# Kernel optimization log

Hardware: AMD Instinct MI355X
Metric: run time of the kernel (lower is better)

Reference implementation:

```python
import jax, jax.numpy as jnp
import numpy as np

NUM_HEADS = 16


def setup_inputs() -> dict:
    key = jax.random.key(0)
    ks = jax.random.split(key, 5)
    B, S, D = 2, 2048, 1024
    scale = 0.02
    return {
        "x": jax.random.normal(ks[0], (B, S, D), dtype=jnp.float32),
        "Wq": jax.random.normal(ks[1], (D, D), dtype=jnp.float32) * scale,
        "Wk": jax.random.normal(ks[2], (D, D), dtype=jnp.float32) * scale,
        "Wv": jax.random.normal(ks[3], (D, D), dtype=jnp.float32) * scale,
        "Wo": jax.random.normal(ks[4], (D, D), dtype=jnp.float32) * scale,
        "bo": jnp.zeros((D,), dtype=jnp.float32),
    }


def reference(x, Wq, Wk, Wv, Wo, bo):
    B, S, D = x.shape
    H = NUM_HEADS
    Dh = D // H
    # project and split heads -> [B, H, S, Dh]
    q = (x @ Wq).reshape(B, S, H, Dh).transpose(0, 2, 1, 3)
    k = (x @ Wk).reshape(B, S, H, Dh).transpose(0, 2, 1, 3)
    v = (x @ Wv).reshape(B, S, H, Dh).transpose(0, 2, 1, 3)
    # full causal attention scores [B, H, S, S]
    scores = jnp.einsum("bhqd,bhkd->bhqk", q, k)
    causal_mask = jnp.triu(jnp.ones((S, S), dtype=bool), k=1)
    scores = jnp.where(causal_mask, -jnp.inf, scores)
    attn = jax.nn.softmax(scores / jnp.sqrt(jnp.float32(Dh)), axis=-1)
    ctx = jnp.einsum("bhqk,bhkd->bhqd", attn, v)
    ctx = ctx.transpose(0, 2, 1, 3).reshape(B, S, D)
    return ctx @ Wo + bo
```

## Files before the change

kernel.cpp:

```cpp
#include <hip/hip_runtime.h>
#include <hip/hip_bf16.h>
#include <math.h>

typedef __bf16 bf16_t;
typedef bf16_t bf16x4 __attribute__((ext_vector_type(4)));
typedef bf16_t bf16x8 __attribute__((ext_vector_type(8)));
typedef float f32x4 __attribute__((ext_vector_type(4)));
typedef unsigned int u32;
typedef u32 u32x2 __attribute__((ext_vector_type(2)));
typedef u32 u32x4 __attribute__((ext_vector_type(4)));

#define MFMA16(a, b, c) __builtin_amdgcn_mfma_f32_16x16x32_bf16(a, b, c, 0, 0, 0)
#define NEG_BIG (-1e30f)
#define QSCALE 0.18033688f

#define GLL16(gp, lp)                                                          \
    __builtin_amdgcn_global_load_lds(                                          \
        (const __attribute__((address_space(1))) unsigned int*)(gp),           \
        (__attribute__((address_space(3))) unsigned int*)(lp), 16, 0, 0)


__global__ __launch_bounds__(256) void prep(const float* __restrict__ x,
                                            const float* __restrict__ Wq,
                                            const float* __restrict__ Wk,
                                            const float* __restrict__ Wv,
                                            const float* __restrict__ Wo,
                                            bf16_t* __restrict__ Xb,
                                            bf16_t* __restrict__ WTqkv,
                                            bf16_t* __restrict__ WoT) {
    __shared__ float tile[32][33];
    const int z = blockIdx.z;
    const int tx = threadIdx.x, ty = threadIdx.y;
    if (z == 4) {
        int i0 = (((blockIdx.y * 32 + blockIdx.x) * 256) + ty * 32 + tx) * 4;
        for (int j = 0; j < 4; j++) {
            int i = i0 + j * 1048576;
            float4 v = *(const float4*)(x + i);
            Xb[i + 0] = (bf16_t)v.x;
            Xb[i + 1] = (bf16_t)v.y;
            Xb[i + 2] = (bf16_t)v.z;
            Xb[i + 3] = (bf16_t)v.w;
        }
    } else {
        const float* W = (z == 0) ? Wq : (z == 1) ? Wk : (z == 2) ? Wv : Wo;
        bf16_t* WT = (z < 3) ? (WTqkv + (size_t)z * 1048576) : WoT;
        int bx = blockIdx.x * 32, by = blockIdx.y * 32;
        for (int i = 0; i < 32; i += 8)
            tile[ty + i][tx] = W[(size_t)(by + ty + i) * 1024 + bx + tx];
        __syncthreads();
        for (int i = 0; i < 32; i += 8)
            WT[(size_t)(bx + ty + i) * 1024 + by + tx] = (bf16_t)tile[tx][ty + i];
    }
}

__global__ __launch_bounds__(256) void gemm_qkv(const bf16_t* __restrict__ X,
                                                const bf16_t* __restrict__ WT,
                                                bf16_t* __restrict__ Qd,
                                                bf16_t* __restrict__ Kd,
                                                bf16_t* __restrict__ Vd) {
    __shared__ bf16_t AsmF[2][128 * 64];
    __shared__ bf16_t BsmF[2][128 * 64];
    const int bid = blockIdx.x;
    const int logical = (bid & 7) * 96 + (bid >> 3);
    const int which = logical >> 8;
    const int rem = logical & 255;
    const bf16_t* Wt = WT + (size_t)which * 1024 * 1024;
    const int bm = (rem >> 3) * 128;
    const int bn = (rem & 7) * 128;
    const int tid = threadIdx.x;
    const int wave = tid >> 6, lane = tid & 63;
    const int wm = (wave >> 1) * 64, wn = (wave & 1) * 64;
    const int col = lane & 15, quad = lane >> 4;
    const int cswz = col & 7;
    const int lr8 = lane >> 3;
    const int jg = (lane & 7) ^ lr8;

    const int srow = wave * 32 + lr8;
    const bf16_t* gA = X  + (size_t)(bm + srow) * 1024 + jg * 8;
    const bf16_t* gB = Wt + (size_t)(bn + srow) * 1024 + jg * 8;

    auto stage = [&](int k0, int bsel) {
        bf16_t* lA = AsmF[bsel] + wave * 2048;
        bf16_t* lB = BsmF[bsel] + wave * 2048;
        for (int j = 0; j < 4; j++) {
            GLL16(gA + (size_t)j * 8192 + k0, lA + j * 512);
            GLL16(gB + (size_t)j * 8192 + k0, lB + j * 512);
        }
    };

    stage(0, 0);

    f32x4 acc[4][4] = {};

    for (int t = 0; t < 16; t++) {
        __syncthreads();
        if (t + 1 < 16) stage((t + 1) * 64, (t + 1) & 1);
        const bf16_t* Ab = AsmF[t & 1];
        const bf16_t* Bb = BsmF[t & 1];
        for (int ks = 0; ks < 2; ks++) {
            bf16x8 af[4], bfr[4];
            for (int mi = 0; mi < 4; mi++)
                af[mi] = *(const bf16x8*)&Ab[(wm + mi * 16 + col) * 64 +
                                             (((ks << 2) + quad) ^ cswz) * 8];
            for (int ni = 0; ni < 4; ni++)
                bfr[ni] = *(const bf16x8*)&Bb[(wn + ni * 16 + col) * 64 +
                                              (((ks << 2) + quad) ^ cswz) * 8];
            if (which != 2) {
                for (int mi = 0; mi < 4; mi++)
                    for (int ni = 0; ni < 4; ni++)
                        acc[mi][ni] = MFMA16(af[mi], bfr[ni], acc[mi][ni]);
            } else {
                for (int mi = 0; mi < 4; mi++)
                    for (int ni = 0; ni < 4; ni++)
                        acc[mi][ni] = MFMA16(bfr[ni], af[mi], acc[mi][ni]);
            }
        }
    }

    if (which != 2) {
        const float sc = (which == 0) ? QSCALE : 1.0f;
        for (int mi = 0; mi < 4; mi++) {
            for (int ni = 0; ni < 4; ni++) {
                int mbase = bm + wm + mi * 16 + quad * 4;
                int n = bn + wn + ni * 16 + col;
                int h = n >> 6, dh = n & 63;
                for (int r = 0; r < 4; r++) {
                    int m = mbase + r;
                    int b = m >> 11, s = m & 2047;
                    size_t bh = (size_t)b * 16 + h;
                    bf16_t val = (bf16_t)(acc[mi][ni][r] * sc);
                    if (which == 0) Qd[(bh * 2048 + s) * 64 + dh] = val;
                    else            Kd[(bh * 2048 + s) * 64 + dh] = val;
                }
            }
        }
    } else {
        for (int mi = 0; mi < 4; mi++) {
            for (int ni = 0; ni < 4; ni++) {
                int nbase = bn + wn + ni * 16 + quad * 4;
                int m = bm + wm + mi * 16 + col;
                int b = m >> 11, s = m & 2047;
                for (int r = 0; r < 4; r++) {
                    int n = nbase + r;
                    int h = n >> 6, dh = n & 63;
                    size_t bh = (size_t)b * 16 + h;
                    Vd[(bh * 64 + dh) * 2048 + s] = (bf16_t)acc[mi][ni][r];
                }
            }
        }
    }
}

__global__ __launch_bounds__(256) void attn(const bf16_t* __restrict__ Q,
                                            const bf16_t* __restrict__ K,
                                            const bf16_t* __restrict__ VT,
                                            bf16_t* __restrict__ CTX) {
    __shared__ __align__(16) bf16_t SMEM[16384];
    bf16_t* KsF = SMEM;
    bf16_t* VsF = SMEM + 8192;

    const int bidx = blockIdx.x;
    const int bh = bidx & 31;
    const int qt = 31 - (bidx >> 5);
    const int tid = threadIdx.x;
    const int wave = tid >> 6, lane = tid & 63;
    const int qhalf = wave & 1, khalf = wave >> 1;
    const int col = lane & 15, quad = lane >> 4;
    const int cswz = col & 7;
    const int lr8 = lane >> 3;
    const int jg = (lane & 7) ^ lr8;

    const bf16_t* Qb = Q + (size_t)bh * 2048 * 64;
    const bf16_t* Kb = K + (size_t)bh * 2048 * 64;
    const bf16_t* Vb = VT + (size_t)bh * 64 * 2048;

    const int strow = wave * 16 + lr8;
    const bf16_t* gK = Kb + (size_t)strow * 64 + jg * 8;
    const bf16_t* gV = Vb + (size_t)strow * 2048 + jg * 8;

    const int b_ = bh >> 4, h_ = bh & 15;

    bf16x8 ones;
    for (int i = 0; i < 8; i++) ones[i] = (bf16_t)1.0f;

    auto stage = [&](int k0, int bsel) {
        bf16_t* lK = KsF + bsel * 4096 + wave * 1024;
        bf16_t* lV = VsF + bsel * 4096 + wave * 1024;
        for (int j = 0; j < 2; j++) {
            GLL16(gK + (size_t)(k0 + j * 8) * 64, lK + j * 512);
            GLL16(gV + (size_t)(k0 + j * 8 * 2048), lV + j * 512);
        }
    };

    stage(0, 0);

    const int q0 = qt * 64;
    const int qrA = q0 + qhalf * 32 + col;
    const bf16x8 qfA0 = *(const bf16x8*)&Qb[(size_t)qrA * 64 + quad * 8];
    const bf16x8 qfA1 = *(const bf16x8*)&Qb[(size_t)qrA * 64 + 32 + quad * 8];
    const bf16x8 qfB0 = *(const bf16x8*)&Qb[(size_t)(qrA + 16) * 64 + quad * 8];
    const bf16x8 qfB1 = *(const bf16x8*)&Qb[(size_t)(qrA + 16) * 64 + 32 + quad * 8];

    f32x4 o[2][4] = {};
    f32x4 accl[2] = {};

    const int iA = (col | ((quad & 1) << 5)) << 2;
    const bool hi = (quad & 2) != 0;

    const int nt = qt + 1;
    for (int g = 0; g < nt; g++) {
        __syncthreads();
        if (g + 1 < nt) stage((g + 1) * 64, (g + 1) & 1);

        const int bsel = g & 1;
        const bf16_t* Kbuf = KsF + bsel * 4096;
        const bf16_t* Vbuf = VsF + bsel * 4096;
        const bool diag = (g == qt);

        u32x2 pwd[2][2];
#pragma unroll
        for (int ksl = 0; ksl < 2; ksl++) {
            const int ksub = khalf * 2 + ksl;
            bf16x8 a0 = *(const bf16x8*)&Kbuf[(ksub * 16 + col) * 64 +
                                              (quad ^ cswz) * 8];
            bf16x8 a1 = *(const bf16x8*)&Kbuf[(ksub * 16 + col) * 64 +
                                              ((4 + quad) ^ cswz) * 8];
#pragma unroll
            for (int G = 0; G < 2; G++) {
                f32x4 z = {};
                z = MFMA16(a0, G ? qfB0 : qfA0, z);
                z = MFMA16(a1, G ? qfB1 : qfA1, z);
                if (diag) {
                    int qloc = qhalf * 32 + G * 16 + col;
                    for (int r = 0; r < 4; r++) {
                        int lk = ksub * 16 + quad * 4 + r;
                        if (lk > qloc) z[r] = NEG_BIG;
                    }
                }
                bf16x4 pw;
#pragma unroll
                for (int r = 0; r < 4; r++)
                    pw[r] = (bf16_t)__builtin_amdgcn_exp2f(z[r]);
                pwd[G][ksl] = __builtin_bit_cast(u32x2, pw);
            }
        }

        bf16x8 vf[4];
#pragma unroll
        for (int d = 0; d < 4; d++)
            vf[d] = *(const bf16x8*)&Vbuf[(d * 16 + col) * 64 +
                                          (((khalf << 2) + quad) ^ cswz) * 8];
#pragma unroll
        for (int G = 0; G < 2; G++) {
            u32x2 sA = pwd[G][0], sB = pwd[G][1];
            int w0a = __builtin_amdgcn_ds_bpermute(iA,      (int)sA.x);
            int w0b = __builtin_amdgcn_ds_bpermute(iA,      (int)sB.x);
            int w1a = __builtin_amdgcn_ds_bpermute(iA,      (int)sA.y);
            int w1b = __builtin_amdgcn_ds_bpermute(iA,      (int)sB.y);
            int w2a = __builtin_amdgcn_ds_bpermute(iA + 64, (int)sA.x);
            int w2b = __builtin_amdgcn_ds_bpermute(iA + 64, (int)sB.x);
            int w3a = __builtin_amdgcn_ds_bpermute(iA + 64, (int)sA.y);
            int w3b = __builtin_amdgcn_ds_bpermute(iA + 64, (int)sB.y);
            u32x4 pu = {(u32)(hi ? w0b : w0a), (u32)(hi ? w1b : w1a),
                        (u32)(hi ? w2b : w2a), (u32)(hi ? w3b : w3a)};
            bf16x8 pf = __builtin_bit_cast(bf16x8, pu);

            accl[G] = MFMA16(pf, ones, accl[G]);
            for (int d = 0; d < 4; d++)
                o[G][d] = MFMA16(pf, vf[d], o[G][d]);
        }
    }

    __syncthreads();
    float* ex = (float*)SMEM;
    if (khalf == 1) {
        float* p = ex + qhalf * 3072 + lane * 48;
#pragma unroll
        for (int G = 0; G < 2; G++)
            for (int d = 0; d < 4; d++)
                *(f32x4*)(p + (G * 4 + d) * 4) = o[G][d];
        *(f32x4*)(p + 32) = accl[0];
        *(f32x4*)(p + 36) = accl[1];
    }
    __syncthreads();
    if (khalf == 0) {
        float* p = ex + qhalf * 3072 + lane * 48;
#pragma unroll
        for (int G = 0; G < 2; G++)
            for (int d = 0; d < 4; d++)
                o[G][d] += *(const f32x4*)(p + (G * 4 + d) * 4);
        accl[0] += *(const f32x4*)(p + 32);
        accl[1] += *(const f32x4*)(p + 36);

#pragma unroll
        for (int G = 0; G < 2; G++) {
            for (int r = 0; r < 4; r++) {
                float rl = __builtin_amdgcn_rcpf(fmaxf(accl[G][r], 1e-20f));
                int s = q0 + qhalf * 32 + G * 16 + quad * 4 + r;
                for (int d = 0; d < 4; d++) {
                    CTX[((size_t)(b_ * 2048 + s)) * 1024 + h_ * 64 + d * 16 + col] =
                        (bf16_t)(o[G][d][r] * rl);
                }
            }
        }
    }
}

__global__ __launch_bounds__(256) void gemm_out(const bf16_t* __restrict__ X,
                                                const bf16_t* __restrict__ WT,
                                                const float* __restrict__ BO,
                                                float* __restrict__ OUT) {
    __shared__ bf16_t AsmF[64 * 64];
    __shared__ bf16_t BsmF[128 * 64];
    const int bid = blockIdx.x;
    const int logical = (bid & 7) * 64 + (bid >> 3);
    const int bm = (logical >> 3) * 64;
    const int bn = (logical & 7) * 128;
    const int tid = threadIdx.x;
    const int wave = tid >> 6, lane = tid & 63;
    const int wm = (wave >> 1) * 32, wn = (wave & 1) * 64;
    const int col = lane & 15, quad = lane >> 4;
    const int cswz = col & 7;
    const int lr8 = lane >> 3;
    const int jg = (lane & 7) ^ lr8;

    const int arow = wave * 16 + lr8;
    const int brow = wave * 32 + lr8;
    const bf16_t* gA = X  + (size_t)(bm + arow) * 1024 + jg * 8;
    const bf16_t* gB = WT + (size_t)(bn + brow) * 1024 + jg * 8;
    bf16_t* lA = AsmF + wave * 1024;
    bf16_t* lB = BsmF + wave * 2048;

    f32x4 acc[2][4] = {};

    for (int k0 = 0; k0 < 1024; k0 += 64) {
        for (int j = 0; j < 2; j++)
            GLL16(gA + (size_t)j * 8192 + k0, lA + j * 512);
        for (int j = 0; j < 4; j++)
            GLL16(gB + (size_t)j * 8192 + k0, lB + j * 512);
        __syncthreads();
        for (int ks = 0; ks < 2; ks++) {
            bf16x8 af[2], bfr[4];
            for (int mi = 0; mi < 2; mi++)
                af[mi] = *(const bf16x8*)&AsmF[(wm + mi * 16 + col) * 64 +
                                               (((ks << 2) + quad) ^ cswz) * 8];
            for (int ni = 0; ni < 4; ni++)
                bfr[ni] = *(const bf16x8*)&BsmF[(wn + ni * 16 + col) * 64 +
                                                (((ks << 2) + quad) ^ cswz) * 8];
            for (int mi = 0; mi < 2; mi++)
                for (int ni = 0; ni < 4; ni++)
                    acc[mi][ni] = MFMA16(af[mi], bfr[ni], acc[mi][ni]);
        }
        __syncthreads();
    }

    for (int mi = 0; mi < 2; mi++) {
        for (int ni = 0; ni < 4; ni++) {
            int mbase = bm + wm + mi * 16 + quad * 4;
            int n = bn + wn + ni * 16 + col;
            float bov = BO[n];
            for (int r = 0; r < 4; r++) {
                int m = mbase + r;
                OUT[(size_t)m * 1024 + n] = acc[mi][ni][r] + bov;
            }
        }
    }
}

extern "C" void kernel_launch(void* const* d_in, const int* in_sizes, int n_in,
                              void* d_out, int out_size, void* d_ws, size_t ws_size,
                              hipStream_t stream) {
    const float* x  = (const float*)d_in[0];
    const float* Wq = (const float*)d_in[1];
    const float* Wk = (const float*)d_in[2];
    const float* Wv = (const float*)d_in[3];
    const float* Wo = (const float*)d_in[4];
    const float* bo = (const float*)d_in[5];
    float* out = (float*)d_out;

    const size_t MEG = 1048576;
    bf16_t* base  = (bf16_t*)d_ws;
    bf16_t* Xb    = base;
    bf16_t* WTqkv = base + 4 * MEG;
    bf16_t* WoT   = base + 7 * MEG;
    bf16_t* Qb    = base + 8 * MEG;
    bf16_t* Kb    = base + 12 * MEG;
    bf16_t* Vb    = base + 16 * MEG;
    bf16_t* Cb    = base + 20 * MEG;

    prep<<<dim3(32, 32, 5), dim3(32, 8), 0, stream>>>(x, Wq, Wk, Wv, Wo,
                                                      Xb, WTqkv, WoT);
    gemm_qkv<<<768, 256, 0, stream>>>(Xb, WTqkv, Qb, Kb, Vb);
    attn<<<1024, 256, 0, stream>>>(Qb, Kb, Vb, Cb);
    gemm_out<<<512, 256, 0, stream>>>(Cb, WoT, bo, out);
}
```

Measured before the change: 172.8 us.

## Double-buffer output GEMM with 128x128 tiles and pad attention reduction scratch

The output projection GEMM moves from 64x128 to 128x128 block tiles with double-buffered LDS stages. The next K-slice's global-to-LDS loads are issued before computing the current one, which overlaps loads with MFMA work and drops one barrier per iteration. The grid halves to 256 blocks, which may underfill the GPU's compute units. Separately, the attention cross-wave reduction scratch uses a 52-float lane stride instead of 48 to reduce LDS bank conflicts.

```diff
diff --git a/kernel.cpp b/kernel.cpp
--- a/kernel.cpp
+++ b/kernel.cpp
@@ -274,7 +274,7 @@
     __syncthreads();
     float* ex = (float*)SMEM;
     if (khalf == 1) {
-        float* p = ex + qhalf * 3072 + lane * 48;
+        float* p = ex + qhalf * 3328 + lane * 52;
 #pragma unroll
         for (int G = 0; G < 2; G++)
             for (int d = 0; d < 4; d++)
@@ -284,7 +284,7 @@
     }
     __syncthreads();
     if (khalf == 0) {
-        float* p = ex + qhalf * 3072 + lane * 48;
+        float* p = ex + qhalf * 3328 + lane * 52;
 #pragma unroll
         for (int G = 0; G < 2; G++)
             for (int d = 0; d < 4; d++)
@@ -310,51 +310,57 @@
                                                 const bf16_t* __restrict__ WT,
                                                 const float* __restrict__ BO,
                                                 float* __restrict__ OUT) {
-    __shared__ bf16_t AsmF[64 * 64];
-    __shared__ bf16_t BsmF[128 * 64];
+    __shared__ bf16_t AsmF[2][128 * 64];
+    __shared__ bf16_t BsmF[2][128 * 64];
     const int bid = blockIdx.x;
-    const int logical = (bid & 7) * 64 + (bid >> 3);
-    const int bm = (logical >> 3) * 64;
+    const int logical = (bid & 7) * 32 + (bid >> 3);
+    const int bm = (logical >> 3) * 128;
     const int bn = (logical & 7) * 128;
     const int tid = threadIdx.x;
     const int wave = tid >> 6, lane = tid & 63;
-    const int wm = (wave >> 1) * 32, wn = (wave & 1) * 64;
+    const int wm = (wave >> 1) * 64, wn = (wave & 1) * 64;
     const int col = lane & 15, quad = lane >> 4;
     const int cswz = col & 7;
     const int lr8 = lane >> 3;
     const int jg = (lane & 7) ^ lr8;
 
-    const int arow = wave * 16 + lr8;
-    const int brow = wave * 32 + lr8;
-    const bf16_t* gA = X  + (size_t)(bm + arow) * 1024 + jg * 8;
-    const bf16_t* gB = WT + (size_t)(bn + brow) * 1024 + jg * 8;
-    bf16_t* lA = AsmF + wave * 1024;
-    bf16_t* lB = BsmF + wave * 2048;
-
-    f32x4 acc[2][4] = {};
-
-    for (int k0 = 0; k0 < 1024; k0 += 64) {
-        for (int j = 0; j < 2; j++)
+    const int srow = wave * 32 + lr8;
+    const bf16_t* gA = X  + (size_t)(bm + srow) * 1024 + jg * 8;
+    const bf16_t* gB = WT + (size_t)(bn + srow) * 1024 + jg * 8;
+
+    auto stage = [&](int k0, int bsel) {
+        bf16_t* lA = AsmF[bsel] + wave * 2048;
+        bf16_t* lB = BsmF[bsel] + wave * 2048;
+        for (int j = 0; j < 4; j++) {
             GLL16(gA + (size_t)j * 8192 + k0, lA + j * 512);
-        for (int j = 0; j < 4; j++)
             GLL16(gB + (size_t)j * 8192 + k0, lB + j * 512);
+        }
+    };
+
+    stage(0, 0);
+
+    f32x4 acc[4][4] = {};
+
+    for (int t = 0; t < 16; t++) {
         __syncthreads();
+        if (t + 1 < 16) stage((t + 1) * 64, (t + 1) & 1);
+        const bf16_t* Ab = AsmF[t & 1];
+        const bf16_t* Bb = BsmF[t & 1];
         for (int ks = 0; ks < 2; ks++) {
-            bf16x8 af[2], bfr[4];
-            for (int mi = 0; mi < 2; mi++)
-                af[mi] = *(const bf16x8*)&AsmF[(wm + mi * 16 + col) * 64 +
-                                               (((ks << 2) + quad) ^ cswz) * 8];
+            bf16x8 af[4], bfr[4];
+            for (int mi = 0; mi < 4; mi++)
+                af[mi] = *(const bf16x8*)&Ab[(wm + mi * 16 + col) * 64 +
+                                             (((ks << 2) + quad) ^ cswz) * 8];
             for (int ni = 0; ni < 4; ni++)
-                bfr[ni] = *(const bf16x8*)&BsmF[(wn + ni * 16 + col) * 64 +
-                                                (((ks << 2) + quad) ^ cswz) * 8];
-            for (int mi = 0; mi < 2; mi++)
+                bfr[ni] = *(const bf16x8*)&Bb[(wn + ni * 16 + col) * 64 +
+                                              (((ks << 2) + quad) ^ cswz) * 8];
+            for (int mi = 0; mi < 4; mi++)
                 for (int ni = 0; ni < 4; ni++)
                     acc[mi][ni] = MFMA16(af[mi], bfr[ni], acc[mi][ni]);
         }
-        __syncthreads();
-    }
-
-    for (int mi = 0; mi < 2; mi++) {
+    }
+
+    for (int mi = 0; mi < 4; mi++) {
         for (int ni = 0; ni < 4; ni++) {
             int mbase = bm + wm + mi * 16 + quad * 4;
             int n = bn + wn + ni * 16 + col;
@@ -392,5 +398,5 @@
                                                       Xb, WTqkv, WoT);
     gemm_qkv<<<768, 256, 0, stream>>>(Xb, WTqkv, Qb, Kb, Vb);
     attn<<<1024, 256, 0, stream>>>(Qb, Kb, Vb, Cb);
-    gemm_out<<<512, 256, 0, stream>>>(Cb, WoT, bo, out);
+    gemm_out<<<256, 256, 0, stream>>>(Cb, WoT, bo, out);
 }
```

New measurement: 180.4 us. 1.04x slower.
